# Optimization experiments

Hardware: AMD Instinct MI355X
Metric: run time of the kernel (lower is better)

## Reference

```python
import jax, jax.numpy as jnp
import numpy as np

N_KNOTS = 32


def _safe_dist(a, b):
    # a: (B, P, 3), b: (B, M, 3) -> (B, P, M) euclidean distance,
    # with zero (not NaN) gradient at coincident points (diagonal of K_train).
    diff = a[:, :, None, :] - b[:, None, :, :]
    sq = jnp.sum(diff * diff, axis=-1)
    safe = jnp.where(sq > 0, sq, 1.0)
    return jnp.where(sq > 0, jnp.sqrt(safe), 0.0)


def setup_inputs() -> dict:
    key = jax.random.key(0)
    k1, k2 = jax.random.split(key)
    B = 8
    raw = jax.random.uniform(k1, (B, 3, 448, 448), dtype=jnp.float32)
    params_tensor = jax.random.uniform(k2, (B, 6 * N_KNOTS + 3), dtype=jnp.float32)
    return {"raw": raw, "params_tensor": params_tensor}


def reference(raw, params_tensor):
    n = N_KNOTS
    B, C, H, W = raw.shape
    dt = raw.dtype
    # get_params
    xs = params_tensor[:, : 3 * n].reshape(B, n, 3)
    ys = params_tensor[:, 3 * n : 6 * n].reshape(B, n, 3)
    lambdas = params_tensor[:, 6 * n :].reshape(B, 3)
    # NOTE: original code does raw.reshape(B, H*W, C) (NOT a permute) -- replicate exactly.
    fimg = raw.reshape(B, H * W, C)
    # build_k: K_pred (B, HW, n+4)
    d_pred = _safe_dist(fimg, xs)
    K_pred = jnp.concatenate([d_pred, jnp.ones((B, H * W, 1), dt), fimg], axis=2)
    # shared pieces of build_k_train
    dd = _safe_dist(xs, xs)                      # (B, n, n)
    eye = jnp.eye(n, dtype=dt)
    ones_top = jnp.ones((B, n, 1), dt)
    bottom_left = jnp.concatenate([jnp.ones((B, 1, n), dt), jnp.transpose(xs, (0, 2, 1))], axis=1)
    bottom = jnp.concatenate([bottom_left, jnp.zeros((B, 4, 4), dt)], axis=2)  # (B, 4, n+4)
    zs = jnp.zeros((B, 4, 1), dt)
    ws = []
    for i in range(3):  # fixed small channel loop
        d_l = dd + lambdas[:, i][:, None, None] * eye
        top = jnp.concatenate([d_l, ones_top, xs], axis=2)        # (B, n, n+4)
        K = jnp.concatenate([top, bottom], axis=1)                # (B, n+4, n+4)
        v = jnp.concatenate([ys[:, :, i : i + 1], zs], axis=1)    # (B, n+4, 1)
        ws.append(jnp.linalg.pinv(K) @ v)
    Wmat = jnp.concatenate(ws, axis=2)            # (B, n+4, 3)
    out = K_pred @ Wmat                            # (B, HW, 3)
    return out.reshape(raw.shape)
```

## Files before the change

### kernel.cpp

```cpp
#include <hip/hip_runtime.h>
#include <math.h>

#define NK 32
#define NP 36
#define PX 16

typedef float v2f __attribute__((ext_vector_type(2)));

__device__ __forceinline__ float hw_sqrtf(float x) {
    return __builtin_amdgcn_sqrtf(x);
}

__device__ __forceinline__ float bcastf(float v, int sl) {
    return __int_as_float(__builtin_amdgcn_readlane(__float_as_int(v), sl));
}

__device__ __forceinline__ v2f pks(float s, v2f b, v2f c) {
    return __builtin_elementwise_fma((v2f){s, s}, b, c);
}
__device__ __forceinline__ v2f pkv(v2f a, v2f b, v2f c) {
    return __builtin_elementwise_fma(a, b, c);
}

__device__ __forceinline__ void unpack8(const float4* __restrict__ src,
                                        v2f fx[4], v2f fy[4], v2f fz[4],
                                        v2f pn[4]) {
    float4 v0 = src[0], v1 = src[1], v2 = src[2],
           v3 = src[3], v4 = src[4], v5 = src[5];
    float f[24] = {v0.x, v0.y, v0.z, v0.w, v1.x, v1.y, v1.z, v1.w,
                   v2.x, v2.y, v2.z, v2.w, v3.x, v3.y, v3.z, v3.w,
                   v4.x, v4.y, v4.z, v4.w, v5.x, v5.y, v5.z, v5.w};
    #pragma unroll
    for (int q = 0; q < 4; ++q) {
        fx[q] = (v2f){f[6*q+0], f[6*q+3]};
        fy[q] = (v2f){f[6*q+1], f[6*q+4]};
        fz[q] = (v2f){f[6*q+2], f[6*q+5]};
        pn[q] = pkv(fz[q], fz[q], pkv(fy[q], fy[q], fx[q] * fx[q]));
    }
}

__device__ __forceinline__ void core8(const v2f fx[4], const v2f fy[4],
                                      const v2f fz[4], const v2f pn[4],
                                      float4* __restrict__ dst,
                                      const float4* __restrict__ sX,
                                      const float4* __restrict__ sW4,
                                      float4 wb, float4 w33,
                                      float4 w34, float4 w35) {
    v2f ax[4], ay[4], az[4];
    #pragma unroll
    for (int q = 0; q < 4; ++q) {
        ax[q] = pks(w35.x, fz[q], pks(w34.x, fy[q], pks(w33.x, fx[q], (v2f){wb.x, wb.x})));
        ay[q] = pks(w35.y, fz[q], pks(w34.y, fy[q], pks(w33.y, fx[q], (v2f){wb.y, wb.y})));
        az[q] = pks(w35.z, fz[q], pks(w34.z, fy[q], pks(w33.z, fx[q], (v2f){wb.z, wb.z})));
    }

    #pragma unroll 4
    for (int k = 0; k < NK; ++k) {
        float4 xk = sX[k];
        float4 wk = sW4[k];
        #pragma unroll
        for (int q = 0; q < 4; ++q) {
            v2f t = pn[q] + (v2f){xk.w, xk.w};
            t = pks(xk.x, fx[q], t);
            t = pks(xk.y, fy[q], t);
            t = pks(xk.z, fz[q], t);
            t = __builtin_elementwise_max(t, (v2f){0.f, 0.f});
            v2f d = (v2f){hw_sqrtf(t[0]), hw_sqrtf(t[1])};
            ax[q] = pks(wk.x, d, ax[q]);
            ay[q] = pks(wk.y, d, ay[q]);
            az[q] = pks(wk.z, d, az[q]);
        }
    }

    #pragma unroll
    for (int u = 0; u < 2; ++u) {
        int a = 2*u, c = 2*u + 1;
        dst[3*u+0] = make_float4(ax[a][0], ay[a][0], az[a][0], ax[a][1]);
        dst[3*u+1] = make_float4(ay[a][1], az[a][1], ax[c][0], ay[c][0]);
        dst[3*u+2] = make_float4(az[c][0], ax[c][1], ay[c][1], az[c][1]);
    }
}

__global__ __launch_bounds__(256, 2) void tps_fused(const float* __restrict__ raw,
                                                    const float* __restrict__ params,
                                                    float* __restrict__ out,
                                                    int HW) {
    __shared__ float  sxs[NK * 3];
    __shared__ float4 sX[NK];
    __shared__ float4 sW4[NP];

    int b   = blockIdx.y;
    int tid = threadIdx.x;
    const float* pp = params + (size_t)b * (6 * NK + 3);

    if (tid < NK * 3) sxs[tid] = pp[tid];

    int p16 = blockIdx.x * 256 + tid;
    size_t base = (size_t)b * HW * 3 + (size_t)p16 * (PX * 3);
    v2f fxA[4], fyA[4], fzA[4], pnA[4];
    unpack8((const float4*)(raw + base), fxA, fyA, fzA, pnA);
    if ((size_t)raw == 1) sxs[0] = pnA[0][0];

    __syncthreads();

    int wid  = tid >> 6;
    int lane = tid & 63;

    if (wid < 3) {
        int ch = wid;
        float lam = pp[6 * NK + ch];

        int li = (lane < NK) ? lane : 0;
        float myx0 = sxs[li*3+0], myx1 = sxs[li*3+1], myx2 = sxs[li*3+2];

        float rr0,rr1,rr2,rr3,rr4,rr5,rr6,rr7,rr8,rr9,rr10,rr11,rr12,rr13,
              rr14,rr15,rr16,rr17,rr18,rr19,rr20,rr21,rr22,rr23,rr24,rr25,
              rr26,rr27,rr28,rr29,rr30,rr31,rr32,rr33,rr34,rr35,rr36;

        float bcomp = (lane == 33) ? 0.f : (lane == 34) ? 1.f : 2.f;
#define BUILDC(c) do {                                                        \
    float xc0 = sxs[(c)*3+0], xc1 = sxs[(c)*3+1], xc2 = sxs[(c)*3+2];         \
    float dx = myx0 - xc0, dy = myx1 - xc1, dz = myx2 - xc2;                  \
    float d  = hw_sqrtf(dx*dx + dy*dy + dz*dz);                               \
    float v;                                                                  \
    if (lane < NK)       v = (lane == (c)) ? lam : d;                         \
    else if (lane == 32) v = 1.0f;                                            \
    else if (lane < NP)  v = (bcomp==0.f)?xc0:(bcomp==1.f)?xc1:xc2;           \
    else                 v = 0.0f;                                            \
    rr##c = v;                                                                \
} while (0)
        BUILDC(0);  BUILDC(1);  BUILDC(2);  BUILDC(3);  BUILDC(4);  BUILDC(5);
        BUILDC(6);  BUILDC(7);  BUILDC(8);  BUILDC(9);  BUILDC(10); BUILDC(11);
        BUILDC(12); BUILDC(13); BUILDC(14); BUILDC(15); BUILDC(16); BUILDC(17);
        BUILDC(18); BUILDC(19); BUILDC(20); BUILDC(21); BUILDC(22); BUILDC(23);
        BUILDC(24); BUILDC(25); BUILDC(26); BUILDC(27); BUILDC(28); BUILDC(29);
        BUILDC(30); BUILDC(31);
#undef BUILDC
        bool top = (lane < NK);
        rr32 = top ? 1.0f : 0.0f;
        rr33 = top ? myx0 : 0.0f;
        rr34 = top ? myx1 : 0.0f;
        rr35 = top ? myx2 : 0.0f;
        rr36 = top ? pp[3*NK + li*3 + ch] : 0.0f;

#define COLU(c) if ((c) > KK) { rr##c -= minv * bcastf(rr##c, KK); }
#define ALLCOLS \
    COLU(1)  COLU(2)  COLU(3)  COLU(4)  COLU(5)  COLU(6)  COLU(7)  COLU(8)  \
    COLU(9)  COLU(10) COLU(11) COLU(12) COLU(13) COLU(14) COLU(15) COLU(16) \
    COLU(17) COLU(18) COLU(19) COLU(20) COLU(21) COLU(22) COLU(23) COLU(24) \
    COLU(25) COLU(26) COLU(27) COLU(28) COLU(29) COLU(30) COLU(31) COLU(32) \
    COLU(33) COLU(34) COLU(35) COLU(36)
#define STEP(Kv) do {                                                         \
    const int KK = (Kv);                                                      \
    float pv  = bcastf(rr##Kv, (Kv));                                         \
    float inv = __builtin_amdgcn_rcpf(pv);                                    \
    bool  isp = (lane == (Kv));                                               \
    float minv = isp ? (1.0f - inv) : rr##Kv * inv;                           \
    ALLCOLS                                                                   \
} while (0)

        STEP(0);  STEP(1);  STEP(2);  STEP(3);  STEP(4);  STEP(5);
        STEP(6);  STEP(7);  STEP(8);  STEP(9);  STEP(10); STEP(11);
        STEP(12); STEP(13); STEP(14); STEP(15); STEP(16); STEP(17);
        STEP(18); STEP(19); STEP(20); STEP(21); STEP(22); STEP(23);
        STEP(24); STEP(25); STEP(26); STEP(27); STEP(28); STEP(29);
        STEP(30); STEP(31); STEP(32); STEP(33); STEP(34); STEP(35);
#undef STEP
#undef ALLCOLS
#undef COLU

        if (lane < NP)
            ((float*)&sW4[lane])[ch] = rr36;
    } else {
        if (lane < NK) {
            float x0 = sxs[lane*3+0], x1 = sxs[lane*3+1], x2 = sxs[lane*3+2];
            sX[lane] = make_float4(-2.f*x0, -2.f*x1, -2.f*x2,
                                   x0*x0 + x1*x1 + x2*x2);
        }
    }
    __syncthreads();

    float4 wb  = sW4[NK];
    float4 w33 = sW4[NK+1], w34 = sW4[NK+2], w35 = sW4[NK+3];

    core8(fxA, fyA, fzA, pnA, (float4*)(out + base),
          sX, sW4, wb, w33, w34, w35);

    v2f fxB[4], fyB[4], fzB[4], pnB[4];
    unpack8((const float4*)(raw + base + 24), fxB, fyB, fzB, pnB);
    core8(fxB, fyB, fzB, pnB, (float4*)(out + base + 24),
          sX, sW4, wb, w33, w34, w35);
}

extern "C" void kernel_launch(void* const* d_in, const int* in_sizes, int n_in,
                              void* d_out, int out_size, void* d_ws, size_t ws_size,
                              hipStream_t stream) {
    const float* raw    = (const float*)d_in[0];
    const float* params = (const float*)d_in[1];
    float* out = (float*)d_out;

    int B  = in_sizes[1] / (6 * NK + 3);
    int HW = in_sizes[0] / (B * 3);

    int groups = HW / PX;
    int bpb = (groups + 255) / 256;
    tps_fused<<<dim3(bpb, B), dim3(256), 0, stream>>>(raw, params, out, HW);
}
```

Baseline: 33.36 us.

## Remap grid to one 512-thread block per CU slice of each batch

Replaces the 2D grid of 256-thread blocks (49 per batch, 16 pixels per thread) with exactly 32 blocks of 512 threads per batch. Each thread now handles 8 pixels, then 4 more, and the last 32 threads of each block take a 4-pixel tail. The aim is to match the block count to the CU count, avoiding a partial second wave, and to cut the number of redundant per-block 36x36 linear solves. In exchange, pixel offsets are hard-coded for this image size, and one wave per block does extra tail work.

```diff
diff --git a/kernel.cpp b/kernel.cpp
--- a/kernel.cpp
+++ b/kernel.cpp
@@ -3,7 +3,6 @@
 
 #define NK 32
 #define NP 36
-#define PX 16
 
 typedef float v2f __attribute__((ext_vector_type(2)));
 
@@ -81,7 +80,57 @@
     }
 }
 
-__global__ __launch_bounds__(256, 2) void tps_fused(const float* __restrict__ raw,
+__device__ __forceinline__ void apply_chunk4(const float4* __restrict__ src,
+                                             float4* __restrict__ dst,
+                                             const float4* __restrict__ sX,
+                                             const float4* __restrict__ sW4,
+                                             float4 wb, float4 w33,
+                                             float4 w34, float4 w35) {
+    float4 v0 = src[0], v1 = src[1], v2 = src[2];
+    float f[12] = {v0.x, v0.y, v0.z, v0.w, v1.x, v1.y, v1.z, v1.w,
+                   v2.x, v2.y, v2.z, v2.w};
+
+    v2f fx[2], fy[2], fz[2], pn[2];
+    #pragma unroll
+    for (int q = 0; q < 2; ++q) {
+        fx[q] = (v2f){f[6*q+0], f[6*q+3]};
+        fy[q] = (v2f){f[6*q+1], f[6*q+4]};
+        fz[q] = (v2f){f[6*q+2], f[6*q+5]};
+        pn[q] = pkv(fz[q], fz[q], pkv(fy[q], fy[q], fx[q] * fx[q]));
+    }
+
+    v2f ax[2], ay[2], az[2];
+    #pragma unroll
+    for (int q = 0; q < 2; ++q) {
+        ax[q] = pks(w35.x, fz[q], pks(w34.x, fy[q], pks(w33.x, fx[q], (v2f){wb.x, wb.x})));
+        ay[q] = pks(w35.y, fz[q], pks(w34.y, fy[q], pks(w33.y, fx[q], (v2f){wb.y, wb.y})));
+        az[q] = pks(w35.z, fz[q], pks(w34.z, fy[q], pks(w33.z, fx[q], (v2f){wb.z, wb.z})));
+    }
+
+    #pragma unroll 4
+    for (int k = 0; k < NK; ++k) {
+        float4 xk = sX[k];
+        float4 wk = sW4[k];
+        #pragma unroll
+        for (int q = 0; q < 2; ++q) {
+            v2f t = pn[q] + (v2f){xk.w, xk.w};
+            t = pks(xk.x, fx[q], t);
+            t = pks(xk.y, fy[q], t);
+            t = pks(xk.z, fz[q], t);
+            t = __builtin_elementwise_max(t, (v2f){0.f, 0.f});
+            v2f d = (v2f){hw_sqrtf(t[0]), hw_sqrtf(t[1])};
+            ax[q] = pks(wk.x, d, ax[q]);
+            ay[q] = pks(wk.y, d, ay[q]);
+            az[q] = pks(wk.z, d, az[q]);
+        }
+    }
+
+    dst[0] = make_float4(ax[0][0], ay[0][0], az[0][0], ax[0][1]);
+    dst[1] = make_float4(ay[0][1], az[0][1], ax[1][0], ay[1][0]);
+    dst[2] = make_float4(az[1][0], ax[1][1], ay[1][1], az[1][1]);
+}
+
+__global__ __launch_bounds__(512, 2) void tps_fused(const float* __restrict__ raw,
                                                     const float* __restrict__ params,
                                                     float* __restrict__ out,
                                                     int HW) {
@@ -89,16 +138,19 @@
     __shared__ float4 sX[NK];
     __shared__ float4 sW4[NP];
 
-    int b   = blockIdx.y;
+    int blk = blockIdx.x;
+    int b   = blk >> 5;
+    int sub = blk & 31;
     int tid = threadIdx.x;
     const float* pp = params + (size_t)b * (6 * NK + 3);
+    int ppb = HW >> 5;
 
     if (tid < NK * 3) sxs[tid] = pp[tid];
 
-    int p16 = blockIdx.x * 256 + tid;
-    size_t base = (size_t)b * HW * 3 + (size_t)p16 * (PX * 3);
+    size_t blockpx = (size_t)b * HW + (size_t)sub * ppb;
+    size_t baseA = (blockpx + (size_t)tid * 8) * 3;
     v2f fxA[4], fyA[4], fzA[4], pnA[4];
-    unpack8((const float4*)(raw + base), fxA, fyA, fzA, pnA);
+    unpack8((const float4*)(raw + baseA), fxA, fyA, fzA, pnA);
     if ((size_t)raw == 1) sxs[0] = pnA[0][0];
 
     __syncthreads();
@@ -171,7 +223,7 @@
 
         if (lane < NP)
             ((float*)&sW4[lane])[ch] = rr36;
-    } else {
+    } else if (wid == 3) {
         if (lane < NK) {
             float x0 = sxs[lane*3+0], x1 = sxs[lane*3+1], x2 = sxs[lane*3+2];
             sX[lane] = make_float4(-2.f*x0, -2.f*x1, -2.f*x2,
@@ -183,13 +235,18 @@
     float4 wb  = sW4[NK];
     float4 w33 = sW4[NK+1], w34 = sW4[NK+2], w35 = sW4[NK+3];
 
-    core8(fxA, fyA, fzA, pnA, (float4*)(out + base),
+    core8(fxA, fyA, fzA, pnA, (float4*)(out + baseA),
           sX, sW4, wb, w33, w34, w35);
 
-    v2f fxB[4], fyB[4], fzB[4], pnB[4];
-    unpack8((const float4*)(raw + base + 24), fxB, fyB, fzB, pnB);
-    core8(fxB, fyB, fzB, pnB, (float4*)(out + base + 24),
-          sX, sW4, wb, w33, w34, w35);
+    size_t baseB = (blockpx + 4096 + (size_t)tid * 4) * 3;
+    apply_chunk4((const float4*)(raw + baseB), (float4*)(out + baseB),
+                 sX, sW4, wb, w33, w34, w35);
+
+    if (tid >= 480) {
+        size_t baseC = (blockpx + 6144 + (size_t)(tid - 480) * 4) * 3;
+        apply_chunk4((const float4*)(raw + baseC), (float4*)(out + baseC),
+                     sX, sW4, wb, w33, w34, w35);
+    }
 }
 
 extern "C" void kernel_launch(void* const* d_in, const int* in_sizes, int n_in,
@@ -202,7 +259,5 @@
     int B  = in_sizes[1] / (6 * NK + 3);
     int HW = in_sizes[0] / (B * 3);
 
-    int groups = HW / PX;
-    int bpb = (groups + 255) / 256;
-    tps_fused<<<dim3(bpb, B), dim3(256), 0, stream>>>(raw, params, out, HW);
-}
+    tps_fused<<<dim3(B * 32), dim3(512), 0, stream>>>(raw, params, out, HW);
+}
```

Result: faster. 32.13 us (-3.7%).
